# Performance work log

Measured on AMD Instinct MI355X. Metric: run time of the kernel, lower is better.

Reference implementation:

```python
import jax, jax.numpy as jnp
import numpy as np

BS, C, A, H, W, D = 4, 64, 4, 16, 16, 16
CIN = C * A          # 256, in_dim
CQK = CIN // 2       # 128


def setup_inputs() -> dict:
    key = jax.random.key(0)
    ks = jax.random.split(key, 9)
    shape = (BS, C, A, H, W, D)
    x = jax.random.normal(ks[0], shape, dtype=jnp.float32)
    g = jax.random.normal(ks[1], shape, dtype=jnp.float32)
    s = 1.0 / np.sqrt(CIN)
    Wq = jax.random.normal(ks[2], (CQK, CIN), dtype=jnp.float32) * s
    bq = jax.random.normal(ks[3], (CQK,), dtype=jnp.float32) * 0.01
    Wk = jax.random.normal(ks[4], (CQK, CIN), dtype=jnp.float32) * s
    bk = jax.random.normal(ks[5], (CQK,), dtype=jnp.float32) * 0.01
    Wv = jax.random.normal(ks[6], (CIN, CIN), dtype=jnp.float32) * s
    bv = jax.random.normal(ks[7], (CIN,), dtype=jnp.float32) * 0.01
    # gamma is nn.Parameter(zeros(1)) at init; use a nonzero value so the
    # attention branch actually contributes to the output.
    gamma = jax.random.normal(ks[8], (1,), dtype=jnp.float32) * 0.1
    return {"x": x, "g": g, "Wq": Wq, "bq": bq, "Wk": Wk, "bk": bk,
            "Wv": Wv, "bv": bv, "gamma": gamma}


def reference(x, g, Wq, bq, Wk, bk, Wv, bv, gamma):
    bs, c, a, h, w, d = x.shape
    n = h * w * d
    xf = x.reshape(bs, c * a, n)          # (bs, CIN, N)
    gf = g.reshape(bs, c * a, n)
    # 1x1 Conv3d == channel matmul
    q = jnp.einsum('oc,bcn->bno', Wq, xf) + bq          # (bs, N, CQK)
    k = jnp.einsum('oc,bcn->bon', Wk, gf) + bk[:, None]  # (bs, CQK, N)
    v = jnp.einsum('oc,bcn->bon', Wv, gf) + bv[:, None]  # (bs, CIN, N)
    energy = jnp.einsum('bno,bom->bnm', q, k)            # (bs, N, N)
    attn = jax.nn.softmax(energy, axis=-1)
    # out[b,c,n] = sum_m v[b,c,m] * attn[b,n,m]
    out = jnp.einsum('bcm,bnm->bcn', v, attn)
    out = out.reshape(bs, c, a, h, w, d)
    return gamma * out + g
```

## Files before the change

### kernel.cpp

```cpp
#include <hip/hip_runtime.h>
#include <stdint.h>

#define NSP   4096
#define SHIFT 44.0f

typedef unsigned short ushort_t;
typedef __attribute__((ext_vector_type(8)))  short short8;
typedef __attribute__((ext_vector_type(16))) float float16;

union U4S8 { uint4 u; short8 s; };

__device__ __forceinline__ unsigned int f2bf_u(float f) {
    unsigned int u = __float_as_uint(f);
    u += 0x7fffu + ((u >> 16) & 1u);
    return u >> 16;
}
__device__ __forceinline__ unsigned short f2bf(float f) { return (unsigned short)f2bf_u(f); }
__device__ __forceinline__ unsigned int packbf(float a, float b) {
    return f2bf_u(a) | (f2bf_u(b) << 16);
}
__device__ __forceinline__ unsigned int cvt_pk_bf16(float a, float b) {
    unsigned int r;
    asm("v_cvt_pk_bf16_f32 %0, %1, %2" : "=v"(r) : "v"(a), "v"(b));
    return r;
}
__device__ __forceinline__ float bf_lo(unsigned int d) { return __uint_as_float(d << 16); }
__device__ __forceinline__ float bf_hi(unsigned int d) { return __uint_as_float(d & 0xffff0000u); }
__device__ __forceinline__ float16 f16zero() {
    float16 v;
    #pragma unroll
    for (int i = 0; i < 16; ++i) v[i] = 0.f;
    return v;
}

__device__ __forceinline__ void gld_lds16(const uint4* g, uint4* l) {
    __builtin_amdgcn_global_load_lds(
        (const __attribute__((address_space(1))) uint32_t*)(uintptr_t)g,
        (__attribute__((address_space(3))) uint32_t*)(uintptr_t)l,
        16, 0, 0);
}

__global__ __launch_bounds__(256) void xgw_prep(
    const float* __restrict__ x, const float* __restrict__ g,
    const float* __restrict__ Wq, const float* __restrict__ Wk,
    const float* __restrict__ Wv,
    ushort_t* __restrict__ Xbf, ushort_t* __restrict__ Gbf,
    ushort_t* __restrict__ Wt)
{
    __shared__ float Ls[256 * 36];

    const int bid = blockIdx.x;
    const int t = threadIdx.x;

    if (bid >= 1024) {
        const int i = ((bid - 1024) * 256 + t) * 8;
        const int o = i >> 8, c = i & 255;
        const float* src; int row;
        if (o < 128)      { src = Wq; row = o; }
        else if (o < 256) { src = Wk; row = o - 128; }
        else              { src = Wv; row = o - 256; }
        const float4 f0 = *(const float4*)(src + row * 256 + c);
        const float4 f1 = *(const float4*)(src + row * 256 + c + 4);
        uint4 pk;
        pk.x = packbf(f0.x, f0.y);
        pk.y = packbf(f0.z, f0.w);
        pk.z = packbf(f1.x, f1.y);
        pk.w = packbf(f1.z, f1.w);
        ((uint4*)Wt)[((o >> 5) * 32 + (c >> 3)) * 32 + (o & 31)] = pk;
        return;
    }

    const float* src = (bid & 1) ? g : x;
    uint4* dst = (uint4*)((bid & 1) ? Gbf : Xbf);
    const int rem = bid >> 1;
    const int b = rem >> 7, chunk = rem & 127;
    const int n0 = chunk << 5;

    #pragma unroll
    for (int i = 0; i < 8; ++i) {
        const int f = t + 256 * i;
        const int c = f >> 3, n4 = (f & 7) * 4;
        const float4 v = *(const float4*)(src + (((b << 8) + c) << 12) + n0 + n4);
        *(float4*)&Ls[c * 36 + n4] = v;
    }
    __syncthreads();
    const int n = t & 31, gs = t >> 5;
    #pragma unroll
    for (int it = 0; it < 4; ++it) {
        const int slot = gs + 8 * it;
        const int cb = slot * 8;
        uint4 pk;
        pk.x = packbf(Ls[(cb + 0) * 36 + n], Ls[(cb + 1) * 36 + n]);
        pk.y = packbf(Ls[(cb + 2) * 36 + n], Ls[(cb + 3) * 36 + n]);
        pk.z = packbf(Ls[(cb + 4) * 36 + n], Ls[(cb + 5) * 36 + n]);
        pk.w = packbf(Ls[(cb + 6) * 36 + n], Ls[(cb + 7) * 36 + n]);
        dst[((b * 128 + chunk) * 32 + slot) * 32 + n] = pk;
    }
}

__global__ __launch_bounds__(256, 2) void qkv_kernel(
    const ushort_t* __restrict__ Xbf, const ushort_t* __restrict__ Gbf,
    const ushort_t* __restrict__ Wt,
    const float* __restrict__ bq, const float* __restrict__ bkp,
    const float* __restrict__ bv,
    ushort_t* __restrict__ Qt, ushort_t* __restrict__ Kt,
    ushort_t* __restrict__ Vt)
{
    const int t = threadIdx.x;
    const int b = blockIdx.x >> 7;
    const int chunk = blockIdx.x & 127;
    const int w = t >> 6, l31 = t & 31, h = (t >> 5) & 1;

    const uint4* A4 = (const uint4*)((w == 0) ? Xbf : Gbf);
    const uint4* W4 = (const uint4*)Wt;
    const int abase = (b * 128 + chunk) * 32;
    const int wrow  = (w == 0) ? 0 : (w == 1) ? 128 : 256 + (w - 2) * 128;
    const int wchunk = wrow >> 5;

    float16 acc[4] = {f16zero(), f16zero(), f16zero(), f16zero()};

    #pragma unroll 2
    for (int ks = 0; ks < 16; ++ks) {
        U4S8 xf; xf.u = A4[(abase + 2 * ks + h) * 32 + l31];
        #pragma unroll
        for (int mt = 0; mt < 4; ++mt) {
            U4S8 wf; wf.u = W4[((wchunk + mt) * 32 + 2 * ks + h) * 32 + l31];
            if (w < 2)
                acc[mt] = __builtin_amdgcn_mfma_f32_32x32x16_bf16(wf.s, xf.s, acc[mt], 0, 0, 0);
            else
                acc[mt] = __builtin_amdgcn_mfma_f32_32x32x16_bf16(xf.s, wf.s, acc[mt], 0, 0, 0);
        }
    }

    if (w < 2) {
        const float* bias = (w == 0) ? bq : bkp;
        uint2* d2 = (uint2*)((w == 0) ? Qt : Kt);
        const int tbase = (b * 128 + chunk) * 16 * 32;
        #pragma unroll
        for (int mt = 0; mt < 4; ++mt) {
            #pragma unroll
            for (int q = 0; q < 4; ++q) {
                const float4 bb = *(const float4*)(bias + mt * 32 + q * 8 + 4 * h);
                uint2 pk2;
                pk2.x = cvt_pk_bf16(acc[mt][4 * q + 0] + bb.x, acc[mt][4 * q + 1] + bb.y);
                pk2.y = cvt_pk_bf16(acc[mt][4 * q + 2] + bb.z, acc[mt][4 * q + 3] + bb.w);
                const int u4i = tbase + (mt * 4 + q) * 32 + l31;
                d2[(size_t)u4i * 2 + h] = pk2;
            }
        }
    } else {
        uint2* v2 = (uint2*)Vt;
        #pragma unroll
        for (int mt = 0; mt < 4; ++mt) {
            const float bb = bv[(w - 2) * 128 + mt * 32 + l31];
            const size_t ub = ((size_t)(b * 8 + (w - 2) * 4 + mt) * 512 + chunk * 4) * 32 + l31;
            #pragma unroll
            for (int q = 0; q < 4; ++q) {
                uint2 pk2;
                pk2.x = cvt_pk_bf16(acc[mt][4 * q + 0] + bb, acc[mt][4 * q + 1] + bb);
                pk2.y = cvt_pk_bf16(acc[mt][4 * q + 2] + bb, acc[mt][4 * q + 3] + bb);
                v2[(ub + (size_t)q * 32) * 2 + h] = pk2;
            }
        }
    }
}

__global__ __launch_bounds__(256, 2) void attn_kernel(
    const ushort_t* __restrict__ Qt, const ushort_t* __restrict__ Kt,
    const ushort_t* __restrict__ Vt,
    ushort_t* __restrict__ Opart, float* __restrict__ lpart)
{
    __shared__ uint4 Klds[2][512];
    __shared__ uint4 Vlds[2][1024];

    const int t    = threadIdx.x;
    const int bid  = blockIdx.x;
    const int xcd  = bid & 7;
    const int slot = bid >> 3;
    const int combo = xcd * 2 + (slot >> 5);
    const int rowblk = slot & 31;
    const int b = combo >> 2, split = combo & 3;
    const int w = t >> 6, l31 = t & 31, h = (t >> 5) & 1;
    const int rg = w & 1, cg = w >> 1;
    const int rowbase = rowblk * 128 + rg * 64;

    const uint4* Q4 = (const uint4*)Qt;
    const uint4* K4 = (const uint4*)Kt;
    const uint4* V4 = (const uint4*)Vt;

    const uint4* Kbase = K4 + (size_t)(b * 128 + split * 32) * 512;
    auto stage = [&](int buf, int kt32) {
        const uint4* ks = Kbase + (size_t)kt32 * 512;
        gld_lds16(ks + t,       &Klds[buf][t]);
        gld_lds16(ks + t + 256, &Klds[buf][t + 256]);
        #pragma unroll
        for (int j = 0; j < 4; ++j) {
            const int idx = t + 256 * j;
            const int c5 = idx >> 7, inner = idx & 127;
            const uint4* vs = V4 + (size_t)((b * 8 + c5) * 512 + split * 128 + kt32 * 4) * 32 + inner;
            gld_lds16(vs, &Vlds[buf][idx]);
        }
    };

    stage(0, 0);

    short8 qf[2][8];
    #pragma unroll
    for (int nt = 0; nt < 2; ++nt) {
        const uint4* Qb = Q4 + (size_t)((b * 128 + rowblk * 4 + rg * 2 + nt) * 16 + h) * 32 + l31;
        #pragma unroll
        for (int ks = 0; ks < 8; ++ks) {
            U4S8 tmp; tmp.u = Qb[ks * 64];
            qf[nt][ks] = tmp.s;
        }
    }

    float16 Oa[2][4];
    #pragma unroll
    for (int nt = 0; nt < 2; ++nt)
        #pragma unroll
        for (int mt = 0; mt < 4; ++mt) Oa[nt][mt] = f16zero();
    float l_i[2] = {0.f, 0.f};

    auto process = [&](const float16& sv, uint4& pfa, uint4& pfb, float& lacc) {
        unsigned int gq[8];
        float ls = 0.f;
        #pragma unroll
        for (int q = 0; q < 4; ++q) {
            const float e0 = __expf(sv[4 * q + 0] - SHIFT);
            const float e1 = __expf(sv[4 * q + 1] - SHIFT);
            const float e2 = __expf(sv[4 * q + 2] - SHIFT);
            const float e3 = __expf(sv[4 * q + 3] - SHIFT);
            ls += (e0 + e1) + (e2 + e3);
            gq[2 * q]     = cvt_pk_bf16(e0, e1);
            gq[2 * q + 1] = cvt_pk_bf16(e2, e3);
        }
        lacc += ls;
        const unsigned int s0a = h ? gq[0] : gq[2];
        const unsigned int s0b = h ? gq[1] : gq[3];
        const unsigned int s1a = h ? gq[4] : gq[6];
        const unsigned int s1b = h ? gq[5] : gq[7];
        const unsigned int r0a = (unsigned int)__shfl_xor((int)s0a, 32);
        const unsigned int r0b = (unsigned int)__shfl_xor((int)s0b, 32);
        const unsigned int r1a = (unsigned int)__shfl_xor((int)s1a, 32);
        const unsigned int r1b = (unsigned int)__shfl_xor((int)s1b, 32);
        pfa = h ? make_uint4(r0a, r0b, gq[2], gq[3]) : make_uint4(gq[0], gq[1], r0a, r0b);
        pfb = h ? make_uint4(r1a, r1b, gq[6], gq[7]) : make_uint4(gq[4], gq[5], r1a, r1b);
    };

    __syncthreads();
    int cur = 0;

    #pragma unroll 1
    for (int kt = 0; kt < 32; ++kt) {
        if (kt < 31) stage(cur ^ 1, kt + 1);

        float16 sA = f16zero(), sB = f16zero();
        #pragma unroll
        for (int ks = 0; ks < 8; ++ks) {
            U4S8 kf; kf.u = Klds[cur][(2 * ks + h) * 32 + l31];
            sA = __builtin_amdgcn_mfma_f32_32x32x16_bf16(kf.s, qf[0][ks], sA, 0, 0, 0);
            sB = __builtin_amdgcn_mfma_f32_32x32x16_bf16(kf.s, qf[1][ks], sB, 0, 0, 0);
        }
        uint4 pf[2][2];
        process(sA, pf[0][0], pf[0][1], l_i[0]);
        process(sB, pf[1][0], pf[1][1], l_i[1]);

        #pragma unroll
        for (int mt = 0; mt < 4; ++mt) {
            #pragma unroll
            for (int ks2 = 0; ks2 < 2; ++ks2) {
                U4S8 vf; vf.u = Vlds[cur][(cg * 4 + mt) * 128 + (ks2 * 2 + h) * 32 + l31];
                U4S8 p0; p0.u = pf[0][ks2];
                U4S8 p1; p1.u = pf[1][ks2];
                Oa[0][mt] = __builtin_amdgcn_mfma_f32_32x32x16_bf16(vf.s, p0.s, Oa[0][mt], 0, 0, 0);
                Oa[1][mt] = __builtin_amdgcn_mfma_f32_32x32x16_bf16(vf.s, p1.s, Oa[1][mt], 0, 0, 0);
            }
        }

        __syncthreads();
        cur ^= 1;
    }

    #pragma unroll
    for (int nt = 0; nt < 2; ++nt) {
        l_i[nt] += __shfl_xor(l_i[nt], 32);
        if (cg == 0 && h == 0)
            lpart[(((split << 2) + b) << 12) + rowbase + nt * 32 + l31] = l_i[nt];
    }
    ushort_t* Ob = Opart + (size_t)(((split << 2) + b) << 8) * NSP;
    #pragma unroll
    for (int mt = 0; mt < 4; ++mt) {
        #pragma unroll
        for (int r = 0; r < 16; ++r) {
            const int c = cg * 128 + mt * 32 + (r & 3) + 8 * (r >> 2) + 4 * h;
            ushort_t* row = Ob + ((size_t)c << 12) + rowbase + l31;
            row[0]  = f2bf(Oa[0][mt][r]);
            row[32] = f2bf(Oa[1][mt][r]);
        }
    }
}

__global__ __launch_bounds__(256) void combine_kernel(
    const ushort_t* __restrict__ Opart, const float* __restrict__ lpart,
    const float* __restrict__ g, const float* __restrict__ gamma_p,
    float* __restrict__ out)
{
    const int gi = blockIdx.x * 256 + threadIdx.x;
    const int n8 = gi & 511;
    const int cc = (gi >> 9) & 255;
    const int b  = gi >> 17;
    const float gmm = gamma_p[0];

    float ls[8], os[8];
    #pragma unroll
    for (int j = 0; j < 8; ++j) { ls[j] = 0.f; os[j] = 0.f; }
    const float4* lp4 = (const float4*)lpart;
    const uint4*  op4 = (const uint4*)Opart;
    #pragma unroll
    for (int s = 0; s < 4; ++s) {
        const int sb = (s << 2) + b;
        const float4 la = lp4[(sb << 10) + n8 * 2];
        const float4 lb = lp4[(sb << 10) + n8 * 2 + 1];
        ls[0] += la.x; ls[1] += la.y; ls[2] += la.z; ls[3] += la.w;
        ls[4] += lb.x; ls[5] += lb.y; ls[6] += lb.z; ls[7] += lb.w;
        const uint4 d = op4[(size_t)(((sb << 8) + cc) << 9) + n8];
        os[0] += bf_lo(d.x); os[1] += bf_hi(d.x);
        os[2] += bf_lo(d.y); os[3] += bf_hi(d.y);
        os[4] += bf_lo(d.z); os[5] += bf_hi(d.z);
        os[6] += bf_lo(d.w); os[7] += bf_hi(d.w);
    }
    const size_t idx = ((size_t)(((b << 8) + cc)) << 12) + n8 * 8;
    const float4 g0 = *(const float4*)(g + idx);
    const float4 g1 = *(const float4*)(g + idx + 4);
    float4 o0, o1;
    o0.x = os[0] * (gmm / ls[0]) + g0.x;
    o0.y = os[1] * (gmm / ls[1]) + g0.y;
    o0.z = os[2] * (gmm / ls[2]) + g0.z;
    o0.w = os[3] * (gmm / ls[3]) + g0.w;
    o1.x = os[4] * (gmm / ls[4]) + g1.x;
    o1.y = os[5] * (gmm / ls[5]) + g1.y;
    o1.z = os[6] * (gmm / ls[6]) + g1.z;
    o1.w = os[7] * (gmm / ls[7]) + g1.w;
    *(float4*)(out + idx)     = o0;
    *(float4*)(out + idx + 4) = o1;
}

extern "C" void kernel_launch(void* const* d_in, const int* in_sizes, int n_in,
                              void* d_out, int out_size, void* d_ws, size_t ws_size,
                              hipStream_t stream)
{
    (void)in_sizes; (void)n_in; (void)out_size; (void)ws_size;
    const float* x     = (const float*)d_in[0];
    const float* g     = (const float*)d_in[1];
    const float* Wq    = (const float*)d_in[2];
    const float* bq    = (const float*)d_in[3];
    const float* Wk    = (const float*)d_in[4];
    const float* bk    = (const float*)d_in[5];
    const float* Wv    = (const float*)d_in[6];
    const float* bv    = (const float*)d_in[7];
    const float* gamma = (const float*)d_in[8];
    float* out = (float*)d_out;

    char* ws = (char*)d_ws;
    ushort_t* Opart = (ushort_t*)(ws);
    ushort_t* Xbf   = (ushort_t*)(ws);
    ushort_t* Gbf   = (ushort_t*)(ws + (8ull  << 20));
    ushort_t* Qt    = (ushort_t*)(ws + (32ull << 20));
    ushort_t* Kt    = (ushort_t*)(ws + (36ull << 20));
    ushort_t* Vt    = (ushort_t*)(ws + (40ull << 20));
    ushort_t* Wt    = (ushort_t*)(ws + (48ull << 20));
    float*    lpart = (float*)   (ws + (48ull << 20) + (256u << 10));

    xgw_prep<<<1088, 256, 0, stream>>>(x, g, Wq, Wk, Wv, Xbf, Gbf, Wt);
    qkv_kernel<<<512, 256, 0, stream>>>(Xbf, Gbf, Wt, bq, bk, bv, Qt, Kt, Vt);
    attn_kernel<<<512, 256, 0, stream>>>(Qt, Kt, Vt, Opart, lpart);
    combine_kernel<<<2048, 256, 0, stream>>>(Opart, lpart, g, gamma, out);
}
```

Before: 229.0 us.

## Fuse x/g bf16 conversion into QKV projection kernel via shared memory

Moves the fp32-to-bf16 transpose/convert of x and g out of the prep kernel and into the QKV projection kernel. Each block stages its own 32-column chunk through LDS into bf16 fragment layout, so the Xbf/Gbf workspace round trip through global memory goes away and the prep kernel only converts the weights. It also swaps the software bf16 rounding for the hardware cvt_pk instruction in the weight conversion and the staging path. In the attention kernel the hardware instruction is replaced by software packbf, which costs extra ALU work there. The extra LDS and barriers in the QKV kernel may cut occupancy.

```diff
diff --git a/kernel.cpp b/kernel.cpp
--- a/kernel.cpp
+++ b/kernel.cpp
@@ -40,80 +40,82 @@
         16, 0, 0);
 }
 
-__global__ __launch_bounds__(256) void xgw_prep(
+__global__ __launch_bounds__(256) void w_prep(
+    const float* __restrict__ Wq, const float* __restrict__ Wk,
+    const float* __restrict__ Wv, ushort_t* __restrict__ Wt)
+{
+    const int t = threadIdx.x;
+    const int i = (blockIdx.x * 256 + t) * 8;
+    const int o = i >> 8, c = i & 255;
+    const float* src; int row;
+    if (o < 128)      { src = Wq; row = o; }
+    else if (o < 256) { src = Wk; row = o - 128; }
+    else              { src = Wv; row = o - 256; }
+    const float4 f0 = *(const float4*)(src + row * 256 + c);
+    const float4 f1 = *(const float4*)(src + row * 256 + c + 4);
+    uint4 pk;
+    pk.x = cvt_pk_bf16(f0.x, f0.y);
+    pk.y = cvt_pk_bf16(f0.z, f0.w);
+    pk.z = cvt_pk_bf16(f1.x, f1.y);
+    pk.w = cvt_pk_bf16(f1.z, f1.w);
+    ((uint4*)Wt)[((o >> 5) * 32 + (c >> 3)) * 32 + (o & 31)] = pk;
+}
+
+__global__ __launch_bounds__(256, 2) void qkvf_kernel(
     const float* __restrict__ x, const float* __restrict__ g,
-    const float* __restrict__ Wq, const float* __restrict__ Wk,
-    const float* __restrict__ Wv,
-    ushort_t* __restrict__ Xbf, ushort_t* __restrict__ Gbf,
-    ushort_t* __restrict__ Wt)
-{
-    __shared__ float Ls[256 * 36];
-
-    const int bid = blockIdx.x;
-    const int t = threadIdx.x;
-
-    if (bid >= 1024) {
-        const int i = ((bid - 1024) * 256 + t) * 8;
-        const int o = i >> 8, c = i & 255;
-        const float* src; int row;
-        if (o < 128)      { src = Wq; row = o; }
-        else if (o < 256) { src = Wk; row = o - 128; }
-        else              { src = Wv; row = o - 256; }
-        const float4 f0 = *(const float4*)(src + row * 256 + c);
-        const float4 f1 = *(const float4*)(src + row * 256 + c + 4);
-        uint4 pk;
-        pk.x = packbf(f0.x, f0.y);
-        pk.y = packbf(f0.z, f0.w);
-        pk.z = packbf(f1.x, f1.y);
-        pk.w = packbf(f1.z, f1.w);
-        ((uint4*)Wt)[((o >> 5) * 32 + (c >> 3)) * 32 + (o & 31)] = pk;
-        return;
-    }
-
-    const float* src = (bid & 1) ? g : x;
-    uint4* dst = (uint4*)((bid & 1) ? Gbf : Xbf);
-    const int rem = bid >> 1;
-    const int b = rem >> 7, chunk = rem & 127;
-    const int n0 = chunk << 5;
-
-    #pragma unroll
-    for (int i = 0; i < 8; ++i) {
-        const int f = t + 256 * i;
-        const int c = f >> 3, n4 = (f & 7) * 4;
-        const float4 v = *(const float4*)(src + (((b << 8) + c) << 12) + n0 + n4);
-        *(float4*)&Ls[c * 36 + n4] = v;
-    }
-    __syncthreads();
-    const int n = t & 31, gs = t >> 5;
-    #pragma unroll
-    for (int it = 0; it < 4; ++it) {
-        const int slot = gs + 8 * it;
-        const int cb = slot * 8;
-        uint4 pk;
-        pk.x = packbf(Ls[(cb + 0) * 36 + n], Ls[(cb + 1) * 36 + n]);
-        pk.y = packbf(Ls[(cb + 2) * 36 + n], Ls[(cb + 3) * 36 + n]);
-        pk.z = packbf(Ls[(cb + 4) * 36 + n], Ls[(cb + 5) * 36 + n]);
-        pk.w = packbf(Ls[(cb + 6) * 36 + n], Ls[(cb + 7) * 36 + n]);
-        dst[((b * 128 + chunk) * 32 + slot) * 32 + n] = pk;
-    }
-}
-
-__global__ __launch_bounds__(256, 2) void qkv_kernel(
-    const ushort_t* __restrict__ Xbf, const ushort_t* __restrict__ Gbf,
     const ushort_t* __restrict__ Wt,
     const float* __restrict__ bq, const float* __restrict__ bkp,
     const float* __restrict__ bv,
     ushort_t* __restrict__ Qt, ushort_t* __restrict__ Kt,
     ushort_t* __restrict__ Vt)
 {
+    __shared__ float Ls[128 * 36];
+    __shared__ uint4 Af[1024];
+    __shared__ uint4 Gf[1024];
+
     const int t = threadIdx.x;
     const int b = blockIdx.x >> 7;
     const int chunk = blockIdx.x & 127;
+    const int n0 = chunk << 5;
     const int w = t >> 6, l31 = t & 31, h = (t >> 5) & 1;
-
-    const uint4* A4 = (const uint4*)((w == 0) ? Xbf : Gbf);
+    const int n = t & 31, gs = t >> 5;
+
+    auto stage_tensor = [&](const float* src, uint4* dst) {
+        float4 rv[8];
+        #pragma unroll
+        for (int i = 0; i < 8; ++i) {
+            const int f = t + 256 * i;
+            const int c = f >> 3, n4 = (f & 7) * 4;
+            rv[i] = *(const float4*)(src + (((b << 8) + c) << 12) + n0 + n4);
+        }
+        #pragma unroll
+        for (int hh = 0; hh < 2; ++hh) {
+            #pragma unroll
+            for (int i = 0; i < 4; ++i) {
+                const int f = t + 256 * (hh * 4 + i);
+                const int cl = (f >> 3) - hh * 128, n4 = (f & 7) * 4;
+                *(float4*)&Ls[cl * 36 + n4] = rv[hh * 4 + i];
+            }
+            __syncthreads();
+            #pragma unroll
+            for (int it = 0; it < 2; ++it) {
+                const int sl = gs + 8 * it;
+                const int cb = sl * 8;
+                uint4 pk;
+                pk.x = cvt_pk_bf16(Ls[(cb + 0) * 36 + n], Ls[(cb + 1) * 36 + n]);
+                pk.y = cvt_pk_bf16(Ls[(cb + 2) * 36 + n], Ls[(cb + 3) * 36 + n]);
+                pk.z = cvt_pk_bf16(Ls[(cb + 4) * 36 + n], Ls[(cb + 5) * 36 + n]);
+                pk.w = cvt_pk_bf16(Ls[(cb + 6) * 36 + n], Ls[(cb + 7) * 36 + n]);
+                dst[(hh * 16 + sl) * 32 + n] = pk;
+            }
+            __syncthreads();
+        }
+    };
+    stage_tensor(x, Af);
+    stage_tensor(g, Gf);
+
+    const uint4* Asrc = (w == 0) ? Af : Gf;
     const uint4* W4 = (const uint4*)Wt;
-    const int abase = (b * 128 + chunk) * 32;
     const int wrow  = (w == 0) ? 0 : (w == 1) ? 128 : 256 + (w - 2) * 128;
     const int wchunk = wrow >> 5;
 
@@ -121,7 +123,7 @@
 
     #pragma unroll 2
     for (int ks = 0; ks < 16; ++ks) {
-        U4S8 xf; xf.u = A4[(abase + 2 * ks + h) * 32 + l31];
+        U4S8 xf; xf.u = Asrc[(2 * ks + h) * 32 + l31];
         #pragma unroll
         for (int mt = 0; mt < 4; ++mt) {
             U4S8 wf; wf.u = W4[((wchunk + mt) * 32 + 2 * ks + h) * 32 + l31];
@@ -232,8 +234,8 @@
             const float e2 = __expf(sv[4 * q + 2] - SHIFT);
             const float e3 = __expf(sv[4 * q + 3] - SHIFT);
             ls += (e0 + e1) + (e2 + e3);
-            gq[2 * q]     = cvt_pk_bf16(e0, e1);
-            gq[2 * q + 1] = cvt_pk_bf16(e2, e3);
+            gq[2 * q]     = packbf(e0, e1);
+            gq[2 * q + 1] = packbf(e2, e3);
         }
         lacc += ls;
         const unsigned int s0a = h ? gq[0] : gq[2];
@@ -364,16 +366,14 @@
 
     char* ws = (char*)d_ws;
     ushort_t* Opart = (ushort_t*)(ws);
-    ushort_t* Xbf   = (ushort_t*)(ws);
-    ushort_t* Gbf   = (ushort_t*)(ws + (8ull  << 20));
     ushort_t* Qt    = (ushort_t*)(ws + (32ull << 20));
     ushort_t* Kt    = (ushort_t*)(ws + (36ull << 20));
     ushort_t* Vt    = (ushort_t*)(ws + (40ull << 20));
     ushort_t* Wt    = (ushort_t*)(ws + (48ull << 20));
     float*    lpart = (float*)   (ws + (48ull << 20) + (256u << 10));
 
-    xgw_prep<<<1088, 256, 0, stream>>>(x, g, Wq, Wk, Wv, Xbf, Gbf, Wt);
-    qkv_kernel<<<512, 256, 0, stream>>>(Xbf, Gbf, Wt, bq, bk, bv, Qt, Kt, Vt);
+    w_prep<<<64, 256, 0, stream>>>(Wq, Wk, Wv, Wt);
+    qkvf_kernel<<<512, 256, 0, stream>>>(x, g, Wt, bq, bk, bv, Qt, Kt, Vt);
     attn_kernel<<<512, 256, 0, stream>>>(Qt, Kt, Vt, Opart, lpart);
     combine_kernel<<<2048, 256, 0, stream>>>(Opart, lpart, g, gamma, out);
 }
```

Result: faster. 211.3 us (-7.7%).
